# Optimization experiments

Hardware: AMD Instinct MI355X
Metric: run time of the kernel (lower is better)

## Reference

```python
import jax, jax.numpy as jnp
import numpy as np

EMBED_DIM = 1024
NUM_HEADS = 16
HEAD_DIM = EMBED_DIM // NUM_HEADS


def _rope_tables(seq_len, dim, dtype):
    # inv_freq over even indices of head_dim
    inv_freq = 1.0 / (10000.0 ** (jnp.arange(0, dim, 2, dtype=jnp.float32) / dim))
    t = jnp.arange(seq_len, dtype=jnp.float32)
    freqs = jnp.einsum('i,j->ij', t, inv_freq)            # [S, dim/2]
    emb = jnp.concatenate([freqs, freqs], axis=-1)        # [S, dim]
    return jnp.cos(emb).astype(dtype)[None], jnp.sin(emb).astype(dtype)[None]  # [1,S,dim]


def _rotate_half(x):
    x1, x2 = jnp.split(x, 2, axis=-1)
    return jnp.concatenate([-x2, x1], axis=-1)


def _apply_rope(x, cos, sin):
    return x * cos + _rotate_half(x) * sin


def setup_inputs() -> dict:
    key = jax.random.key(0)
    ks = jax.random.split(key, 9)
    S, B, E = 2048, 2, EMBED_DIM
    sc = 1.0 / np.sqrt(E)
    inp = {
        'query': jax.random.normal(ks[0], (S, B, E), jnp.float32),
        'Wq': jax.random.normal(ks[1], (E, E), jnp.float32) * sc,
        'bq': jnp.zeros((E,), jnp.float32),
        'Wk': jax.random.normal(ks[2], (E, E), jnp.float32) * sc,
        'bk': jnp.zeros((E,), jnp.float32),
        'Wv': jax.random.normal(ks[3], (E, E), jnp.float32) * sc,
        'bv': jnp.zeros((E,), jnp.float32),
        'Wo': jax.random.normal(ks[4], (E, E), jnp.float32) * sc,
        'bo': jnp.zeros((E,), jnp.float32),
    }
    return inp


def reference(query, Wq, bq, Wk, bk, Wv, bv, Wo, bo):
    tgt_len, bsz, E = query.shape
    H, hd = NUM_HEADS, HEAD_DIM
    scaling = hd ** (-0.5)

    # self-attention projections (torch Linear: x @ W.T + b)
    q = (query @ Wq.T + bq) * scaling
    k = query @ Wk.T + bk
    v = query @ Wv.T + bv

    # [S, B, E] -> [B*H, S, hd]
    def to_heads(x):
        return x.reshape(tgt_len, bsz * H, hd).transpose(1, 0, 2)

    q, k, v = to_heads(q), to_heads(k), to_heads(v)

    cos, sin = _rope_tables(tgt_len, hd, q.dtype)  # [1,S,hd]
    q = _apply_rope(q, cos, sin)
    k = _apply_rope(k, cos, sin)

    attn_weights = jnp.einsum('bqd,bkd->bqk', q, k)       # [B*H, S, S]
    attn_probs = jax.nn.softmax(attn_weights, axis=-1)
    attn = jnp.einsum('bqk,bkd->bqd', attn_probs, v)      # [B*H, S, hd]

    attn = attn.transpose(1, 0, 2).reshape(tgt_len, bsz, E)
    return attn @ Wo.T + bo
```

## Files before the change

### kernel.cpp

```cpp
#include <hip/hip_runtime.h>
#include <hip/hip_bf16.h>


typedef short shortx8 __attribute__((ext_vector_type(8)));
typedef float floatx4 __attribute__((ext_vector_type(4)));
typedef float floatx16 __attribute__((ext_vector_type(16)));

#define S_LEN 2048
#define BATCH 2
#define EMB 1024
#define NH 16
#define HD 64
#define BH 32
#define MROWS 4096
#define HEAD_STRIDE (S_LEN*HD)

#define QSCALE 0.1803368801111204f

#if __has_builtin(__builtin_amdgcn_exp2f)
#define EXP2(x) __builtin_amdgcn_exp2f(x)
#else
#define EXP2(x) exp2f(x)
#endif

__device__ __forceinline__ float b2f(unsigned short u) {
    union { unsigned int i; float f; } v; v.i = ((unsigned int)u) << 16; return v.f;
}
__device__ __forceinline__ unsigned short f2b(float f) {
    union { float f; unsigned int i; } v; v.f = f;
    unsigned int x = v.i;
    return (unsigned short)((x + 0x7fffu + ((x >> 16) & 1u)) >> 16);
}
__device__ __forceinline__ unsigned int fbits(float f) {
    union { float f; unsigned int i; } v; v.f = f; return v.i;
}
__device__ __forceinline__ unsigned int pack_bf16_2(float lo, float hi) {
    return __builtin_amdgcn_perm(fbits(hi) + 0x8000u, fbits(lo) + 0x8000u, 0x07060302u);
}
__device__ __forceinline__ unsigned int cvtpk_bf16(float lo, float hi) {
    unsigned int r;
    asm("v_cvt_pk_bf16_f32 %0, %1, %2" : "=v"(r) : "v"(lo), "v"(hi));
    return r;
}
__device__ __forceinline__ void plswap(unsigned int &a, unsigned int &b) {
#if __has_builtin(__builtin_amdgcn_permlane32_swap)
    {
        auto r = __builtin_amdgcn_permlane32_swap(a, b, false, false);
        a = r[0]; b = r[1];
    }
#else
    asm volatile("v_permlane32_swap_b32 %0, %1" : "+v"(a), "+v"(b));
#endif
}
__device__ __forceinline__ shortx8 cvt8(const float* p) {
    floatx4 a = *(const floatx4*)p;
    floatx4 b = *(const floatx4*)(p + 4);
    shortx8 r;
    r[0] = (short)f2b(a[0]); r[1] = (short)f2b(a[1]);
    r[2] = (short)f2b(a[2]); r[3] = (short)f2b(a[3]);
    r[4] = (short)f2b(b[0]); r[5] = (short)f2b(b[1]);
    r[6] = (short)f2b(b[2]); r[7] = (short)f2b(b[3]);
    return r;
}
__device__ __forceinline__ shortx8 cvt8f(const float* p) {
    floatx4 a = *(const floatx4*)p;
    floatx4 b = *(const floatx4*)(p + 4);
    union { uint4 u; shortx8 s; } r;
    r.u.x = pack_bf16_2(a[0], a[1]);
    r.u.y = pack_bf16_2(a[2], a[3]);
    r.u.z = pack_bf16_2(b[0], b[1]);
    r.u.w = pack_bf16_2(b[2], b[3]);
    return r.s;
}
__device__ __forceinline__ void g2l16(const unsigned short* g, unsigned short* l) {
    __builtin_amdgcn_global_load_lds(
        (const __attribute__((address_space(1))) unsigned int*)(const void*)g,
        (__attribute__((address_space(3))) unsigned int*)(void*)l, 16, 0, 0);
}

__global__ __launch_bounds__(256) void prep(
    const float* __restrict__ X,
    const float* __restrict__ Wq, const float* __restrict__ Wk,
    const float* __restrict__ Wv,
    unsigned short* __restrict__ Xb, unsigned short* __restrict__ Wb,
    float* __restrict__ rtab)
{
    const int g = blockIdx.x * 256 + threadIdx.x;
    if (g < 65536) {
        const int s = g >> 5, j = g & 31;
        const float inv = expf(-(float)j * (9.210340371976184f / 32.0f));
        const float ang = (float)s * inv;
        rtab[s * 64 + j]      = cosf(ang);
        rtab[s * 64 + 32 + j] = sinf(ang);
    } else if (g < 458752) {
        const int h = g - 65536;
        const int seg = h >> 17;
        const int idx = (h & 131071) * 8;
        const float* W = (seg == 0) ? Wq : (seg == 1) ? Wk : Wv;
        *(shortx8*)&Wb[seg * 1048576 + idx] = cvt8(&W[idx]);
    } else {
        const int idx = (g - 458752) * 8;
        *(shortx8*)&Xb[idx] = cvt8(&X[idx]);
    }
}

__device__ __forceinline__ void qkv_epilogue(
    floatx4 (&acc)[4][4], int mat, int m0, int nn0, int wm, int wn,
    int qm, int quad, const float* bias, const float* rtab,
    unsigned short* dst)
{
    if (mat == 2) {
#pragma unroll
        for (int i = 0; i < 4; i++) {
#pragma unroll
            for (int j = 0; j < 4; j++) {
                const int colg = nn0 + wn + j * 16 + qm;
                const float bv_ = bias[colg];
                const int h = colg >> 6, d = colg & 63;
#pragma unroll
                for (int r = 0; r < 4; r++) {
                    const int rowg = m0 + wm + i * 16 + quad * 4 + r;
                    const int s = rowg >> 1, b = rowg & 1;
                    dst[((b * NH + h) * HD + d) * S_LEN + s] = f2b(acc[i][j][r] + bv_);
                }
            }
        }
    } else {
        const float scale = (mat == 0) ? QSCALE : 1.0f;
#pragma unroll
        for (int i = 0; i < 4; i++) {
#pragma unroll
            for (int jp = 0; jp < 2; jp++) {
                const int c1 = nn0 + wn + jp * 16 + qm;
                const float b1 = bias[c1], b2 = bias[c1 + 32];
                const int h = c1 >> 6;
                const int d1 = c1 & 63;
#pragma unroll
                for (int r = 0; r < 4; r++) {
                    const int rowg = m0 + wm + i * 16 + quad * 4 + r;
                    const int s = rowg >> 1, b = rowg & 1;
                    const float cs = rtab[s * 64 + d1];
                    const float sn = rtab[s * 64 + d1 + 32];
                    const float x1 = (acc[i][jp][r] + b1) * scale;
                    const float x2 = (acc[i][jp + 2][r] + b2) * scale;
                    unsigned short* base = &dst[((b * NH + h) * S_LEN + s) * HD];
                    base[d1]      = f2b(x1 * cs - x2 * sn);
                    base[d1 + 32] = f2b(x2 * cs + x1 * sn);
                }
            }
        }
    }
}

__global__ __launch_bounds__(256) void qkv_gemm_gl(
    const unsigned short* __restrict__ Xb,
    const unsigned short* __restrict__ Wb,
    const float* __restrict__ bq, const float* __restrict__ bk,
    const float* __restrict__ bv,
    const float* __restrict__ rtab,
    unsigned short* __restrict__ Qh, unsigned short* __restrict__ Kh,
    unsigned short* __restrict__ Vt)
{
    __shared__ unsigned short At[128 * 64];
    __shared__ unsigned short Bt[128 * 64];

    const int tid  = threadIdx.x;
    const int wave = tid >> 6, lane = tid & 63;
    const int wm = (wave >> 1) * 64, wn = (wave & 1) * 64;
    const int qm = lane & 15, quad = lane >> 4;

    const int m0  = blockIdx.x * 128;
    const int n0g = blockIdx.y * 128;
    const int mat = n0g >> 10;
    const int nn0 = n0g & 1023;

    const unsigned short* W = Wb + (size_t)mat * 1048576;
    const float* bias = (mat == 0) ? bq : (mat == 1) ? bk : bv;
    unsigned short* dst = (mat == 0) ? Qh : (mat == 1) ? Kh : Vt;

    floatx4 acc[4][4] = {};

    const int xs = qm & 7;

    for (int k0 = 0; k0 < EMB; k0 += 64) {
#pragma unroll
        for (int c = 0; c < 4; c++) {
            const int e   = (c * 256 + tid) * 8;
            const int row = e >> 6;
            const int gcol = (((e >> 3) & 7) ^ (row & 7)) * 8;
            g2l16(&Xb[(m0 + row) * EMB + k0 + gcol], &At[e]);
            g2l16(&W[(nn0 + row) * EMB + k0 + gcol], &Bt[e]);
        }
        __syncthreads();

#pragma unroll
        for (int kk = 0; kk < 2; kk++) {
            shortx8 a[4], b[4];
#pragma unroll
            for (int i = 0; i < 4; i++)
                a[i] = *(shortx8*)&At[(wm + i * 16 + qm) * 64 + (((kk * 4 + quad) ^ xs) * 8)];
#pragma unroll
            for (int j = 0; j < 4; j++)
                b[j] = *(shortx8*)&Bt[(wn + j * 16 + qm) * 64 + (((kk * 4 + quad) ^ xs) * 8)];
#pragma unroll
            for (int i = 0; i < 4; i++)
#pragma unroll
                for (int j = 0; j < 4; j++)
                    acc[i][j] = __builtin_amdgcn_mfma_f32_16x16x32_bf16(a[i], b[j], acc[i][j], 0, 0, 0);
        }
        __syncthreads();
    }

    qkv_epilogue(acc, mat, m0, nn0, wm, wn, qm, quad, bias, rtab, dst);
}

#define LDB 72

__global__ __launch_bounds__(256) void qkv_gemm_fb(
    const float* __restrict__ X,
    const unsigned short* __restrict__ Wb,
    const float* __restrict__ bq, const float* __restrict__ bk,
    const float* __restrict__ bv,
    const float* __restrict__ rtab,
    unsigned short* __restrict__ Qh, unsigned short* __restrict__ Kh,
    unsigned short* __restrict__ Vt)
{
    __shared__ unsigned short At[128 * LDB];
    __shared__ unsigned short Bt[128 * LDB];

    const int tid  = threadIdx.x;
    const int wave = tid >> 6, lane = tid & 63;
    const int wm = (wave >> 1) * 64, wn = (wave & 1) * 64;
    const int qm = lane & 15, quad = lane >> 4;

    const int m0  = blockIdx.x * 128;
    const int n0g = blockIdx.y * 128;
    const int mat = n0g >> 10;
    const int nn0 = n0g & 1023;

    const unsigned short* W = Wb + (size_t)mat * 1048576;
    const float* bias = (mat == 0) ? bq : (mat == 1) ? bk : bv;
    unsigned short* dst = (mat == 0) ? Qh : (mat == 1) ? Kh : Vt;

    const int r0 = tid >> 3;
    const int ko = (tid & 7) * 8;

    floatx4 acc[4][4] = {};

    for (int k0 = 0; k0 < EMB; k0 += 64) {
#pragma unroll
        for (int c = 0; c < 4; c++) {
            const int row = r0 + 32 * c;
            *(shortx8*)&At[row * LDB + ko] = cvt8(&X[(m0 + row) * EMB + k0 + ko]);
            *(shortx8*)&Bt[row * LDB + ko] = *(const shortx8*)&W[(nn0 + row) * EMB + k0 + ko];
        }
        __syncthreads();

#pragma unroll
        for (int kk = 0; kk < 2; kk++) {
            shortx8 a[4], b[4];
#pragma unroll
            for (int i = 0; i < 4; i++)
                a[i] = *(shortx8*)&At[(wm + i * 16 + qm) * LDB + kk * 32 + quad * 8];
#pragma unroll
            for (int j = 0; j < 4; j++)
                b[j] = *(shortx8*)&Bt[(wn + j * 16 + qm) * LDB + kk * 32 + quad * 8];
#pragma unroll
            for (int i = 0; i < 4; i++)
#pragma unroll
                for (int j = 0; j < 4; j++)
                    acc[i][j] = __builtin_amdgcn_mfma_f32_16x16x32_bf16(a[i], b[j], acc[i][j], 0, 0, 0);
        }
        __syncthreads();
    }

    qkv_epilogue(acc, mat, m0, nn0, wm, wn, qm, quad, bias, rtab, dst);
}

#define SW8(c8, r) ((((c8) ^ ((r) & 7))) * 8)

__global__ __launch_bounds__(512, 4) void attn_kernel(
    unsigned short* Qh,
    const unsigned short* __restrict__ Kh,
    const unsigned short* __restrict__ Vt)
{
    __shared__ __align__(16) unsigned short lds[8192 + 8192 + 512];
    unsigned short* ldsK  = lds;
    unsigned short* ldsVT = lds + 8192;

    const int tid  = threadIdx.x;
    const int wave = tid >> 6, lane = tid & 63;
    const int l32 = lane & 31, half = lane >> 5;
    const int qg = wave >> 1, ks = wave & 1;
    const int bh = blockIdx.y;
    const int qrow = blockIdx.x * 128 + qg * 32;

    unsigned short* Qp = Qh + bh * HEAD_STRIDE;
    const unsigned short* Kp = Kh + bh * HEAD_STRIDE;
    const unsigned short* Vp = Vt + bh * HEAD_STRIDE;

    shortx8 aq[4];
#pragma unroll
    for (int kk = 0; kk < 4; kk++)
        aq[kk] = *(const shortx8*)&Qp[(qrow + l32) * HD + kk * 16 + half * 8];

    floatx16 od0 = {}, od1 = {};
    float l_run = 0.0f;

    const int kb = ks * 64;

    const int kr = tid >> 3, kc8 = tid & 7;
    const int vr = tid >> 4, vc8 = tid & 15;

    shortx8 rk0 = *(const shortx8*)&Kp[kr * HD + kc8 * 8];
    shortx8 rk1 = *(const shortx8*)&Kp[(kr + 64) * HD + kc8 * 8];
    shortx8 rv0 = *(const shortx8*)&Vp[vr * S_LEN + vc8 * 8];
    shortx8 rv1 = *(const shortx8*)&Vp[(vr + 32) * S_LEN + vc8 * 8];

    for (int kt = 0; kt < S_LEN / 128; kt++) {
        *(shortx8*)&ldsK[kr * 64 + SW8(kc8, kr)]        = rk0;
        *(shortx8*)&ldsK[(kr + 64) * 64 + SW8(kc8, kr)] = rk1;
        *(shortx8*)&ldsVT[vr * 128 + SW8(vc8, vr)]        = rv0;
        *(shortx8*)&ldsVT[(vr + 32) * 128 + SW8(vc8, vr)] = rv1;
        __syncthreads();

        if (kt + 1 < S_LEN / 128) {
            const int nb = (kt + 1) * 128;
            rk0 = *(const shortx8*)&Kp[(nb + kr) * HD + kc8 * 8];
            rk1 = *(const shortx8*)&Kp[(nb + kr + 64) * HD + kc8 * 8];
            rv0 = *(const shortx8*)&Vp[vr * S_LEN + nb + vc8 * 8];
            rv1 = *(const shortx8*)&Vp[(vr + 32) * S_LEN + nb + vc8 * 8];
        }

#pragma unroll
        for (int sub = 0; sub < 2; sub++) {
            floatx16 sc = {};
#pragma unroll
            for (int kk = 0; kk < 4; kk++) {
                const shortx8 kf = *(shortx8*)&ldsK[
                    (kb + sub * 32 + l32) * 64 + SW8(kk * 2 + half, l32)];
                sc = __builtin_amdgcn_mfma_f32_32x32x16_bf16(kf, aq[kk], sc, 0, 0, 0);
            }
            float p[16];
#pragma unroll
            for (int g = 0; g < 16; g++) p[g] = EXP2(sc[g]);
#pragma unroll
            for (int c = 0; c < 4; c++)
                l_run += (p[4 * c] + p[4 * c + 1]) + (p[4 * c + 2] + p[4 * c + 3]);

#pragma unroll
            for (int f = 0; f < 2; f++) {
                unsigned int d0 = cvtpk_bf16(p[8 * f + 0], p[8 * f + 1]);
                unsigned int d2 = cvtpk_bf16(p[8 * f + 4], p[8 * f + 5]);
                plswap(d0, d2);
                unsigned int d1 = cvtpk_bf16(p[8 * f + 2], p[8 * f + 3]);
                unsigned int d3 = cvtpk_bf16(p[8 * f + 6], p[8 * f + 7]);
                plswap(d1, d3);
                union { unsigned int u[4]; shortx8 s; } fr;
                fr.u[0] = d0; fr.u[1] = d1; fr.u[2] = d2; fr.u[3] = d3;

                const int c8 = (kb >> 3) + (sub * 2 + f) * 2 + half;
                const shortx8 v0 = *(shortx8*)&ldsVT[l32 * 128 + SW8(c8, l32)];
                const shortx8 v1 = *(shortx8*)&ldsVT[(32 + l32) * 128 + SW8(c8, l32)];
                od0 = __builtin_amdgcn_mfma_f32_32x32x16_bf16(fr.s, v0, od0, 0, 0, 0);
                od1 = __builtin_amdgcn_mfma_f32_32x32x16_bf16(fr.s, v1, od1, 0, 0, 0);
            }
        }
        __syncthreads();
    }

    l_run += __shfl_xor(l_run, 32, 64);

    float* ltab  = (float*)(lds + 16384) + qg * 64 + ks * 32;
    float* odbuf = (float*)lds + qg * 2048;
    if (half == 0) ltab[l32] = l_run;
    if (ks == 1) {
#pragma unroll
        for (int g = 0; g < 16; g++) {
            const int row = (g & 3) + 8 * (g >> 2) + 4 * half;
            odbuf[row * 64 + l32]      = od0[g];
            odbuf[row * 64 + 32 + l32] = od1[g];
        }
    }
    __syncthreads();
    if (ks == 0) {
        const float* l0 = (float*)(lds + 16384) + qg * 64;
        const float* l1 = l0 + 32;
#pragma unroll
        for (int g = 0; g < 16; g++) {
            const int row = (g & 3) + 8 * (g >> 2) + 4 * half;
            const float inv = 1.0f / (l0[row] + l1[row]);
            const float v0 = od0[g] + odbuf[row * 64 + l32];
            const float v1 = od1[g] + odbuf[row * 64 + 32 + l32];
            Qp[(qrow + row) * HD + l32]      = f2b(v0 * inv);
            Qp[(qrow + row) * HD + 32 + l32] = f2b(v1 * inv);
        }
    }
}

__global__ __launch_bounds__(256) void out_gemm(
    const unsigned short* __restrict__ O,
    const float* __restrict__ Wo, const float* __restrict__ bo,
    float* __restrict__ out)
{
    __shared__ unsigned short At[128 * LDB];
    __shared__ unsigned short Bt[64 * LDB];

    const int tid  = threadIdx.x;
    const int wave = tid >> 6, lane = tid & 63;
    const int wm = (wave >> 1) * 64, wn = (wave & 1) * 32;
    const int qm = lane & 15, quad = lane >> 4;
    const int m0 = blockIdx.x * 128;
    const int n0 = blockIdx.y * 64;

    const int r0 = tid >> 3;
    const int ko = (tid & 7) * 8;

    floatx4 acc[4][2] = {};

    for (int k0 = 0; k0 < EMB; k0 += 64) {
        const int k = k0 + ko;
#pragma unroll
        for (int c = 0; c < 4; c++) {
            const int row = r0 + 32 * c;
            const int m = m0 + row;
            *(shortx8*)&At[row * LDB + ko] =
                *(const shortx8*)&O[(((m & 1) * NH + (k >> 6)) * S_LEN + (m >> 1)) * HD + (k & 63)];
        }
#pragma unroll
        for (int c = 0; c < 2; c++) {
            const int row = r0 + 32 * c;
            *(shortx8*)&Bt[row * LDB + ko] = cvt8f(&Wo[(n0 + row) * EMB + k]);
        }
        __syncthreads();

#pragma unroll
        for (int kk = 0; kk < 2; kk++) {
            shortx8 a[4], b[2];
#pragma unroll
            for (int i = 0; i < 4; i++)
                a[i] = *(shortx8*)&At[(wm + i * 16 + qm) * LDB + kk * 32 + quad * 8];
#pragma unroll
            for (int j = 0; j < 2; j++)
                b[j] = *(shortx8*)&Bt[(wn + j * 16 + qm) * LDB + kk * 32 + quad * 8];
#pragma unroll
            for (int i = 0; i < 4; i++)
#pragma unroll
                for (int j = 0; j < 2; j++)
                    acc[i][j] = __builtin_amdgcn_mfma_f32_16x16x32_bf16(a[i], b[j], acc[i][j], 0, 0, 0);
        }
        __syncthreads();
    }

#pragma unroll
    for (int i = 0; i < 4; i++) {
#pragma unroll
        for (int j = 0; j < 2; j++) {
            const int colg = n0 + wn + j * 16 + qm;
            const float bv_ = bo[colg];
#pragma unroll
            for (int r = 0; r < 4; r++) {
                const int rowg = m0 + wm + i * 16 + quad * 4 + r;
                out[rowg * EMB + colg] = acc[i][j][r] + bv_;
            }
        }
    }
}

extern "C" void kernel_launch(void* const* d_in, const int* in_sizes, int n_in,
                              void* d_out, int out_size, void* d_ws, size_t ws_size,
                              hipStream_t stream) {
    const float* X  = (const float*)d_in[0];
    const float* Wq = (const float*)d_in[1];
    const float* bq = (const float*)d_in[2];
    const float* Wk = (const float*)d_in[3];
    const float* bk = (const float*)d_in[4];
    const float* Wv = (const float*)d_in[5];
    const float* bv = (const float*)d_in[6];
    const float* Wo = (const float*)d_in[7];
    const float* bo = (const float*)d_in[8];
    float* out = (float*)d_out;

    unsigned short* ws = (unsigned short*)d_ws;
    unsigned short* Vt  = ws;
    unsigned short* Qh  = ws + (size_t)BH * HEAD_STRIDE;
    unsigned short* Xb  = ws + (size_t)2 * BH * HEAD_STRIDE;
    unsigned short* Kh  = (unsigned short*)d_out;
    unsigned short* Wb  = (unsigned short*)d_out + 4194304;
    float*          Rt  = (float*)d_out + 3670016;

    const bool use_xb = ws_size >= (size_t)24 * 1024 * 1024;

    prep<<<dim3(use_xb ? 3840 : 1792), 256, 0, stream>>>(X, Wq, Wk, Wv, Xb, Wb, Rt);

    if (use_xb)
        qkv_gemm_gl<<<dim3(MROWS / 128, 3 * EMB / 128), 256, 0, stream>>>(
            Xb, Wb, bq, bk, bv, Rt, Qh, Kh, Vt);
    else
        qkv_gemm_fb<<<dim3(MROWS / 128, 3 * EMB / 128), 256, 0, stream>>>(
            X, Wb, bq, bk, bv, Rt, Qh, Kh, Vt);

    attn_kernel<<<dim3(S_LEN / 128, BH), 512, 0, stream>>>(Qh, Kh, Vt);
    out_gemm<<<dim3(MROWS / 128, EMB / 64), 256, 0, stream>>>(Qh, Wo, bo, out);
}
```

Baseline: 199.6 us.

## Double-buffer QKV GEMM LDS tiles and register-prefetch output GEMM loads

The QKV projection GEMM now uses two LDS buffers, issuing direct global-to-LDS loads for the next K tile while MFMAs consume the current one. The output projection GEMM preloads the next K tile of O and Wo into registers during the current tile's compute, then converts and stores to LDS. Both aim to hide global memory latency behind matrix math. In exchange, LDS use doubles to 64KB in the QKV kernel, which may lower occupancy, and the output GEMM holds more registers.

```diff
diff --git a/kernel.cpp b/kernel.cpp
--- a/kernel.cpp
+++ b/kernel.cpp
@@ -152,7 +152,7 @@
     }
 }
 
-__global__ __launch_bounds__(256) void qkv_gemm_gl(
+__global__ __launch_bounds__(256) void qkv_gemm_db(
     const unsigned short* __restrict__ Xb,
     const unsigned short* __restrict__ Wb,
     const float* __restrict__ bq, const float* __restrict__ bk,
@@ -161,8 +161,7 @@
     unsigned short* __restrict__ Qh, unsigned short* __restrict__ Kh,
     unsigned short* __restrict__ Vt)
 {
-    __shared__ unsigned short At[128 * 64];
-    __shared__ unsigned short Bt[128 * 64];
+    __shared__ unsigned short sm[32768];
 
     const int tid  = threadIdx.x;
     const int wave = tid >> 6, lane = tid & 63;
@@ -182,26 +181,41 @@
 
     const int xs = qm & 7;
 
-    for (int k0 = 0; k0 < EMB; k0 += 64) {
-#pragma unroll
-        for (int c = 0; c < 4; c++) {
-            const int e   = (c * 256 + tid) * 8;
-            const int row = e >> 6;
-            const int gcol = (((e >> 3) & 7) ^ (row & 7)) * 8;
-            g2l16(&Xb[(m0 + row) * EMB + k0 + gcol], &At[e]);
-            g2l16(&W[(nn0 + row) * EMB + k0 + gcol], &Bt[e]);
-        }
-        __syncthreads();
+#pragma unroll
+    for (int c = 0; c < 4; c++) {
+        const int e   = (c * 256 + tid) * 8;
+        const int row = e >> 6;
+        const int gcol = (((e >> 3) & 7) ^ (row & 7)) * 8;
+        g2l16(&Xb[(m0 + row) * EMB + gcol], &sm[e]);
+        g2l16(&W[(nn0 + row) * EMB + gcol], &sm[8192 + e]);
+    }
+    __syncthreads();
+
+    for (int t = 0; t < 16; ++t) {
+        const int cur = (t & 1) << 14;
+        const int nxt = ((t + 1) & 1) << 14;
+
+        if (t + 1 < 16) {
+            const int k0 = (t + 1) * 64;
+#pragma unroll
+            for (int c = 0; c < 4; c++) {
+                const int e   = (c * 256 + tid) * 8;
+                const int row = e >> 6;
+                const int gcol = (((e >> 3) & 7) ^ (row & 7)) * 8;
+                g2l16(&Xb[(m0 + row) * EMB + k0 + gcol], &sm[nxt + e]);
+                g2l16(&W[(nn0 + row) * EMB + k0 + gcol], &sm[nxt + 8192 + e]);
+            }
+        }
 
 #pragma unroll
         for (int kk = 0; kk < 2; kk++) {
             shortx8 a[4], b[4];
 #pragma unroll
             for (int i = 0; i < 4; i++)
-                a[i] = *(shortx8*)&At[(wm + i * 16 + qm) * 64 + (((kk * 4 + quad) ^ xs) * 8)];
+                a[i] = *(shortx8*)&sm[cur + (wm + i * 16 + qm) * 64 + (((kk * 4 + quad) ^ xs) * 8)];
 #pragma unroll
             for (int j = 0; j < 4; j++)
-                b[j] = *(shortx8*)&Bt[(wn + j * 16 + qm) * 64 + (((kk * 4 + quad) ^ xs) * 8)];
+                b[j] = *(shortx8*)&sm[cur + 8192 + (wn + j * 16 + qm) * 64 + (((kk * 4 + quad) ^ xs) * 8)];
 #pragma unroll
             for (int i = 0; i < 4; i++)
 #pragma unroll
@@ -418,21 +432,53 @@
 
     floatx4 acc[4][2] = {};
 
+    shortx8 ra[4];
+    floatx4 rb[2][2];
+
+    {
+        const int k = ko;
+#pragma unroll
+        for (int c = 0; c < 4; c++) {
+            const int m = m0 + r0 + 32 * c;
+            ra[c] = *(const shortx8*)&O[(((m & 1) * NH + (k >> 6)) * S_LEN + (m >> 1)) * HD + (k & 63)];
+        }
+#pragma unroll
+        for (int c = 0; c < 2; c++) {
+            const float* wp = &Wo[(n0 + r0 + 32 * c) * EMB + k];
+            rb[c][0] = *(const floatx4*)wp;
+            rb[c][1] = *(const floatx4*)(wp + 4);
+        }
+    }
+
     for (int k0 = 0; k0 < EMB; k0 += 64) {
-        const int k = k0 + ko;
-#pragma unroll
-        for (int c = 0; c < 4; c++) {
-            const int row = r0 + 32 * c;
-            const int m = m0 + row;
-            *(shortx8*)&At[row * LDB + ko] =
-                *(const shortx8*)&O[(((m & 1) * NH + (k >> 6)) * S_LEN + (m >> 1)) * HD + (k & 63)];
-        }
+#pragma unroll
+        for (int c = 0; c < 4; c++)
+            *(shortx8*)&At[(r0 + 32 * c) * LDB + ko] = ra[c];
 #pragma unroll
         for (int c = 0; c < 2; c++) {
-            const int row = r0 + 32 * c;
-            *(shortx8*)&Bt[row * LDB + ko] = cvt8f(&Wo[(n0 + row) * EMB + k]);
-        }
-        __syncthreads();
+            union { uint4 u; shortx8 s; } r;
+            r.u.x = pack_bf16_2(rb[c][0][0], rb[c][0][1]);
+            r.u.y = pack_bf16_2(rb[c][0][2], rb[c][0][3]);
+            r.u.z = pack_bf16_2(rb[c][1][0], rb[c][1][1]);
+            r.u.w = pack_bf16_2(rb[c][1][2], rb[c][1][3]);
+            *(shortx8*)&Bt[(r0 + 32 * c) * LDB + ko] = r.s;
+        }
+        __syncthreads();
+
+        if (k0 + 64 < EMB) {
+            const int k = k0 + 64 + ko;
+#pragma unroll
+            for (int c = 0; c < 4; c++) {
+                const int m = m0 + r0 + 32 * c;
+                ra[c] = *(const shortx8*)&O[(((m & 1) * NH + (k >> 6)) * S_LEN + (m >> 1)) * HD + (k & 63)];
+            }
+#pragma unroll
+            for (int c = 0; c < 2; c++) {
+                const float* wp = &Wo[(n0 + r0 + 32 * c) * EMB + k];
+                rb[c][0] = *(const floatx4*)wp;
+                rb[c][1] = *(const floatx4*)(wp + 4);
+            }
+        }
 
 #pragma unroll
         for (int kk = 0; kk < 2; kk++) {
@@ -494,7 +540,7 @@
     prep<<<dim3(use_xb ? 3840 : 1792), 256, 0, stream>>>(X, Wq, Wk, Wv, Xb, Wb, Rt);
 
     if (use_xb)
-        qkv_gemm_gl<<<dim3(MROWS / 128, 3 * EMB / 128), 256, 0, stream>>>(
+        qkv_gemm_db<<<dim3(MROWS / 128, 3 * EMB / 128), 256, 0, stream>>>(
             Xb, Wb, bq, bk, bv, Rt, Qh, Kh, Vt);
     else
         qkv_gemm_fb<<<dim3(MROWS / 128, 3 * EMB / 128), 256, 0, stream>>>(
```

After: 185.3 us, median of 3. -7.2%, faster.
